# Kernel optimization log

Measured on AMD Instinct MI355X. Metric: run time of the kernel, lower is better.

The kernel has to match this reference:

```python
import jax, jax.numpy as jnp
import numpy as np

EMBED = 1024
N_HEADS = 16
HEAD_DIM = EMBED // N_HEADS
B, T = 2, 2048


def setup_inputs() -> dict:
    key = jax.random.key(0)
    k1, k2, k3 = jax.random.split(key, 3)
    x = jax.random.normal(k1, (B, T, EMBED), dtype=jnp.float32)
    # torch nn.Linear(embed, 3*embed, bias=False): weight [3C, C]; store as [C, 3C] for x @ W
    w_attn = jax.random.normal(k2, (EMBED, 3 * EMBED), dtype=jnp.float32) * (EMBED ** -0.5)
    w_proj = jax.random.normal(k3, (EMBED, EMBED), dtype=jnp.float32) * (EMBED ** -0.5)
    return {"x": x, "w_attn": w_attn, "w_proj": w_proj}


def reference(x, w_attn, w_proj):
    Bb, Tt, C = x.shape
    kqv = x @ w_attn  # [B, T, 3C]
    # NOTE: original code unpacks as k, q, v (k first)
    k, q, v = jnp.split(kqv, 3, axis=2)
    def heads(t):
        return t.reshape(Bb, Tt, N_HEADS, HEAD_DIM).transpose(0, 2, 1, 3)  # [B, H, T, D]
    k, q, v = heads(k), heads(q), heads(v)
    scale = HEAD_DIM ** -0.5
    wei = jnp.einsum("bhqd,bhkd->bhqk", q, k) * scale  # [B, H, T, T]
    mask = jnp.tril(jnp.ones((Tt, Tt), dtype=bool))
    wei = jnp.where(mask[None, None], wei, -jnp.inf)
    wei = jax.nn.softmax(wei, axis=-1)
    y = jnp.einsum("bhqk,bhkd->bhqd", wei, v)  # [B, H, T, D]
    y = y.transpose(0, 2, 1, 3).reshape(Bb, Tt, C)
    return y @ w_proj
```

## Files before the change

### kernel.cpp

```cpp
#include <hip/hip_runtime.h>

typedef unsigned short u16;
typedef unsigned int u32;

typedef __attribute__((ext_vector_type(4))) float f32x4;
typedef __attribute__((ext_vector_type(8))) short s16x8;

__device__ __forceinline__ u16 f2bf(float f) {
    u32 u = __builtin_bit_cast(u32, f);
    u += 0x7fffu + ((u >> 16) & 1u);
    return (u16)(u >> 16);
}

__device__ __forceinline__ u32 pk_bf16(float a, float b) {
    return (u32)f2bf(a) | ((u32)f2bf(b) << 16);
}

__device__ __forceinline__ u32 cvtpk(float a, float b) {
    u32 r;
    asm("v_cvt_pk_bf16_f32 %0, %1, %2" : "=v"(r) : "v"(a), "v"(b));
    return r;
}

#if __has_builtin(__builtin_amdgcn_exp2f)
#define EXP2(x) __builtin_amdgcn_exp2f(x)
#else
#define EXP2(x) exp2f(x)
#endif

__device__ __forceinline__ void gload16(const u16* g, u16* l) {
    __builtin_amdgcn_global_load_lds(
        (const __attribute__((address_space(1))) void*)(const void*)g,
        (__attribute__((address_space(3))) void*)(void*)l, 16, 0, 0);
}

__global__ void k_cast(const float* __restrict__ in, u16* __restrict__ out) {
    int i = (blockIdx.x * 256 + threadIdx.x) * 4;
    float4 v = *(const float4*)(in + i);
    uint2 pk;
    pk.x = pk_bf16(v.x, v.y);
    pk.y = pk_bf16(v.z, v.w);
    *(uint2*)(out + i) = pk;
}

__global__ void k_transpose(const float* __restrict__ in, u16* __restrict__ out,
                            int K, int N) {
    __shared__ float tile[32][33];
    int n0 = blockIdx.x * 32, k0 = blockIdx.y * 32;
    int x = threadIdx.x, y = threadIdx.y;
#pragma unroll
    for (int j = 0; j < 32; j += 8)
        tile[y + j][x] = in[(size_t)(k0 + y + j) * N + n0 + x];
    __syncthreads();
#pragma unroll
    for (int j = 0; j < 32; j += 8)
        out[(size_t)(n0 + y + j) * K + k0 + x] = f2bf(tile[x][y + j]);
}

template <int EPI>
__global__ __launch_bounds__(256, 2) void k_gemm(
        const u16* __restrict__ A, const u16* __restrict__ Bt,
        void* __restrict__ Cout, u16* __restrict__ Vt, int N, int K) {
    __shared__ u16 As[128 * 32];
    __shared__ u16 Bs[128 * 32];
    const int nbn = N >> 7;
    const int bm = (int)blockIdx.x / nbn, bn = (int)blockIdx.x % nbn;
    const int tid = threadIdx.x;
    const int wv = tid >> 6, ln = tid & 63;
    const int lg = ln >> 4, lr = ln & 15;
    const int wr = (wv >> 1) << 6, wc = (wv & 1) << 6;

    const u16* gA = A + (size_t)(bm * 128 + wv * 32 + (ln >> 2)) * K + (ln & 3) * 8;
    const u16* gB = Bt + (size_t)(bn * 128 + wv * 32 + (ln >> 2)) * K + (ln & 3) * 8;
    u16* lA = As + wv * 1024;
    u16* lB = Bs + wv * 1024;

    f32x4 acc[4][4] = {};

    for (int k0 = 0; k0 < K; k0 += 32) {
        gload16(gA + k0, lA);
        gload16(gA + k0 + 16 * K, lA + 512);
        gload16(gB + k0, lB);
        gload16(gB + k0 + 16 * K, lB + 512);
        __syncthreads();
        s16x8 af[4], bf[4];
#pragma unroll
        for (int mi = 0; mi < 4; ++mi)
            af[mi] = *(const s16x8*)&As[(wr + mi * 16 + lr) * 32 + lg * 8];
#pragma unroll
        for (int ni = 0; ni < 4; ++ni)
            bf[ni] = *(const s16x8*)&Bs[(wc + ni * 16 + lr) * 32 + lg * 8];
#pragma unroll
        for (int mi = 0; mi < 4; ++mi)
#pragma unroll
            for (int ni = 0; ni < 4; ++ni)
                acc[mi][ni] = __builtin_amdgcn_mfma_f32_16x16x32_bf16(
                        af[mi], bf[ni], acc[mi][ni], 0, 0, 0);
        __syncthreads();
    }

    const int crow0 = bm * 128 + wr + lg * 4;
    const int ccol0 = bn * 128 + wc + lr;
    if (EPI == 0) {
        float* Co = (float*)Cout;
#pragma unroll
        for (int mi = 0; mi < 4; ++mi)
#pragma unroll
            for (int ni = 0; ni < 4; ++ni)
#pragma unroll
                for (int r = 0; r < 4; ++r)
                    Co[(size_t)(crow0 + mi * 16 + r) * N + ccol0 + ni * 16] =
                            acc[mi][ni][r];
    } else {
        if (bn < 16) {
            const float qs = (bn >= 8) ? 0.18033688011112042f : 1.0f;
            u16* Co = (u16*)Cout;
#pragma unroll
            for (int mi = 0; mi < 4; ++mi)
#pragma unroll
                for (int ni = 0; ni < 4; ++ni)
#pragma unroll
                    for (int r = 0; r < 4; ++r)
                        Co[(size_t)(crow0 + mi * 16 + r) * 3072 + ccol0 + ni * 16] =
                                f2bf(acc[mi][ni][r] * qs);
        } else {
#pragma unroll
            for (int mi = 0; mi < 4; ++mi) {
                int row = crow0 + mi * 16;
                int bb = row >> 11, t = row & 2047;
#pragma unroll
                for (int ni = 0; ni < 4; ++ni) {
                    int hd = ccol0 + ni * 16 - 2048;
                    uint2 pk;
                    pk.x = pk_bf16(acc[mi][ni][0], acc[mi][ni][1]);
                    pk.y = pk_bf16(acc[mi][ni][2], acc[mi][ni][3]);
                    *(uint2*)&Vt[(size_t)(bb * 1024 + hd) * 2048 + t] = pk;
                }
            }
        }
    }
}

__global__ __launch_bounds__(256, 2) void k_attn(
        const u16* __restrict__ kqv, const u16* __restrict__ Vt,
        u16* __restrict__ y) {
    const int orig = blockIdx.x;
    const int xcd = orig & 7, slot = orig >> 3;
    const int bh = xcd * 4 + (slot >> 4);
    const int qp = slot & 15;
    const int b = bh >> 4, h = bh & 15;
    const int tid = threadIdx.x;
    const int wave = tid >> 6, lane = tid & 63;
    const int lg = lane >> 4, lr = lane & 15;

    __shared__ u16 Ks[2][64 * 72];
    __shared__ u16 Vs[2][64 * 72];
    __shared__ u16 Ps[4][16 * 64];

    const u16* Kg = kqv + (size_t)b * 2048 * 3072 + h * 64;
    const u16* Qg = Kg + 1024;
    const u16* Vg = Vt + (size_t)bh * 64 * 2048;

    const int srow = tid >> 2, ssl = tid & 3;
    const int soff = srow * 72 + ssl * 8;
    const u16* kgp = Kg + (size_t)srow * 3072 + ssl * 8;
    const u16* vgp = Vg + (size_t)srow * 2048 + ssl * 8;

    s16x8 ones;
#pragma unroll
    for (int i = 0; i < 8; ++i) ones[i] = (short)0x3F80;

    for (int pass = 0; pass < 2; ++pass) {
        const int qt = pass ? (31 - qp) : qp;
        const int nkt = qt + 1;
        const int qbase = qt * 64 + wave * 16;

        const u16* qrp = Qg + (size_t)(qbase + lr) * 3072;
        const s16x8 qf0 = *(const s16x8*)(qrp + lg * 8);
        const s16x8 qf1 = *(const s16x8*)(qrp + 32 + lg * 8);

        f32x4 o[4] = {};
        f32x4 l4 = {};

        uint4 ka0 = *(const uint4*)(kgp);
        uint4 ka1 = *(const uint4*)(kgp + 32);
        uint4 va0 = *(const uint4*)(vgp);
        uint4 va1 = *(const uint4*)(vgp + 32);
        *(uint4*)&Ks[0][soff] = ka0;
        *(uint4*)&Ks[0][soff + 32] = ka1;
        *(uint4*)&Vs[0][soff] = va0;
        *(uint4*)&Vs[0][soff + 32] = va1;

        for (int kt = 0; kt < nkt; ++kt) {
            const int cur = kt & 1;
            __syncthreads();
            const bool more = (kt + 1) < nkt;
            if (more) {
                const u16* kn = kgp + (size_t)(kt + 1) * 64 * 3072;
                const u16* vn = vgp + (kt + 1) * 64;
                ka0 = *(const uint4*)(kn);
                ka1 = *(const uint4*)(kn + 32);
                va0 = *(const uint4*)(vn);
                va1 = *(const uint4*)(vn + 32);
            }

            f32x4 st[4];
#pragma unroll
            for (int kb = 0; kb < 4; ++kb) {
                s16x8 kf0 = *(const s16x8*)&Ks[cur][(kb * 16 + lr) * 72 + lg * 8];
                s16x8 kf1 = *(const s16x8*)&Ks[cur][(kb * 16 + lr) * 72 + 32 + lg * 8];
                f32x4 z = {};
                z = __builtin_amdgcn_mfma_f32_16x16x32_bf16(kf0, qf0, z, 0, 0, 0);
                z = __builtin_amdgcn_mfma_f32_16x16x32_bf16(kf1, qf1, z, 0, 0, 0);
                st[kb] = z;
            }

            if (kt == nkt - 1) {
                const int q_abs = qbase + lr;
                const int kb0 = kt * 64 + lg * 4;
#pragma unroll
                for (int kb = 0; kb < 4; ++kb)
#pragma unroll
                    for (int r = 0; r < 4; ++r)
                        st[kb][r] = EXP2((kb0 + kb * 16 + r <= q_abs)
                                             ? st[kb][r] : -3e38f);
            } else {
#pragma unroll
                for (int kb = 0; kb < 4; ++kb)
#pragma unroll
                    for (int r = 0; r < 4; ++r) st[kb][r] = EXP2(st[kb][r]);
            }

#pragma unroll
            for (int kb = 0; kb < 4; ++kb) {
                const int kbs = (kb + lr) & 3;
                uint2 w;
                w.x = cvtpk(st[kb][0], st[kb][1]);
                w.y = cvtpk(st[kb][2], st[kb][3]);
                *(uint2*)&Ps[wave][lr * 64 + kbs * 16 + lg * 4] = w;
            }
            asm volatile("s_waitcnt lgkmcnt(0)" ::: "memory");
            __builtin_amdgcn_sched_barrier(0);

#pragma unroll
            for (int half = 0; half < 2; ++half) {
                const int kbs = ((half * 2 + (lg >> 1)) + lr) & 3;
                s16x8 pf = *(const s16x8*)&Ps[wave][lr * 64 + kbs * 16 + (lg & 1) * 8];
                l4 = __builtin_amdgcn_mfma_f32_16x16x32_bf16(ones, pf, l4, 0, 0, 0);
#pragma unroll
                for (int dt = 0; dt < 4; ++dt) {
                    s16x8 vf = *(const s16x8*)&Vs[cur][(dt * 16 + lr) * 72 + half * 32 + lg * 8];
                    o[dt] = __builtin_amdgcn_mfma_f32_16x16x32_bf16(vf, pf, o[dt], 0, 0, 0);
                }
            }

            if (more) {
                *(uint4*)&Ks[cur ^ 1][soff] = ka0;
                *(uint4*)&Ks[cur ^ 1][soff + 32] = ka1;
                *(uint4*)&Vs[cur ^ 1][soff] = va0;
                *(uint4*)&Vs[cur ^ 1][soff + 32] = va1;
            }
        }
        __syncthreads();

        const float inv = 1.0f / l4[0];
        u16* yb = y + (size_t)(b * 2048 + qbase + lr) * 1024 + h * 64;
#pragma unroll
        for (int dt = 0; dt < 4; ++dt) {
            uint2 w;
            w.x = cvtpk(o[dt][0] * inv, o[dt][1] * inv);
            w.y = cvtpk(o[dt][2] * inv, o[dt][3] * inv);
            *(uint2*)(yb + dt * 16 + lg * 4) = w;
        }
    }
}

extern "C" void kernel_launch(void* const* d_in, const int* in_sizes, int n_in,
                              void* d_out, int out_size, void* d_ws, size_t ws_size,
                              hipStream_t stream) {
    const float* x = (const float*)d_in[0];
    const float* w_attn = (const float*)d_in[1];
    const float* w_proj = (const float*)d_in[2];
    float* out = (float*)d_out;
    char* ws = (char*)d_ws;

    u16* x_bf = (u16*)(ws);
    u16* wat  = (u16*)(ws + (size_t)(8 << 20));
    u16* wpt  = (u16*)(ws + (size_t)(14 << 20));
    u16* kqv  = (u16*)(ws + (size_t)(16 << 20));
    u16* vt   = (u16*)(ws + (size_t)(40 << 20));
    u16* yb   = (u16*)(ws + (size_t)(48 << 20));

    k_cast<<<4096, 256, 0, stream>>>(x, x_bf);
    k_transpose<<<dim3(96, 32), dim3(32, 8), 0, stream>>>(w_attn, wat, 1024, 3072);
    k_transpose<<<dim3(32, 32), dim3(32, 8), 0, stream>>>(w_proj, wpt, 1024, 1024);
    k_gemm<1><<<32 * 24, 256, 0, stream>>>(x_bf, wat, kqv, vt, 3072, 1024);
    k_attn<<<512, 256, 0, stream>>>(kqv, vt, yb);
    k_gemm<0><<<32 * 8, 256, 0, stream>>>(yb, wpt, out, nullptr, 1024, 1024);
}
```

Measured before the change: 182.2 us.

## Use direct global-to-LDS async loads with XOR swizzle and one q-tile per block

The attention kernel now stages K and V tiles with global_load_lds directly into XOR-swizzled LDS tiles, dropping the register round-trip and the padded layout. Each block handles a single query tile instead of a balanced pair, so the grid doubles and launch bounds allow 4 blocks per CU. Wave priority is raised around the MFMA sections, and the P buffer gets a finer swizzle. The cost is less load balance per block, since causal work is no longer paired inside a block and relies on the scheduler instead. The exp2 builtin is also replaced by exp2f.

```diff
diff --git a/kernel.cpp b/kernel.cpp
--- a/kernel.cpp
+++ b/kernel.cpp
@@ -5,6 +5,7 @@
 
 typedef __attribute__((ext_vector_type(4))) float f32x4;
 typedef __attribute__((ext_vector_type(8))) short s16x8;
+typedef __attribute__((ext_vector_type(4))) short s16x4;
 
 __device__ __forceinline__ u16 f2bf(float f) {
     u32 u = __builtin_bit_cast(u32, f);
@@ -22,11 +23,7 @@
     return r;
 }
 
-#if __has_builtin(__builtin_amdgcn_exp2f)
-#define EXP2(x) __builtin_amdgcn_exp2f(x)
-#else
 #define EXP2(x) exp2f(x)
-#endif
 
 __device__ __forceinline__ void gload16(const u16* g, u16* l) {
     __builtin_amdgcn_global_load_lds(
@@ -141,137 +138,140 @@
     }
 }
 
-__global__ __launch_bounds__(256, 2) void k_attn(
+__global__ __launch_bounds__(256, 4) void k_attn(
         const u16* __restrict__ kqv, const u16* __restrict__ Vt,
         u16* __restrict__ y) {
     const int orig = blockIdx.x;
     const int xcd = orig & 7, slot = orig >> 3;
-    const int bh = xcd * 4 + (slot >> 4);
-    const int qp = slot & 15;
+    const int bh = xcd * 4 + (slot >> 5);
+    const int qs = slot & 31;
+    const int qt = (qs & 1) ? (31 - (qs >> 1)) : (qs >> 1);
     const int b = bh >> 4, h = bh & 15;
     const int tid = threadIdx.x;
     const int wave = tid >> 6, lane = tid & 63;
     const int lg = lane >> 4, lr = lane & 15;
 
-    __shared__ u16 Ks[2][64 * 72];
-    __shared__ u16 Vs[2][64 * 72];
+    __shared__ u16 Ks[2][64 * 64];
+    __shared__ u16 Vs[2][64 * 64];
     __shared__ u16 Ps[4][16 * 64];
 
     const u16* Kg = kqv + (size_t)b * 2048 * 3072 + h * 64;
     const u16* Qg = Kg + 1024;
     const u16* Vg = Vt + (size_t)bh * 64 * 2048;
 
-    const int srow = tid >> 2, ssl = tid & 3;
-    const int soff = srow * 72 + ssl * 8;
-    const u16* kgp = Kg + (size_t)srow * 3072 + ssl * 8;
-    const u16* vgp = Vg + (size_t)srow * 2048 + ssl * 8;
+    const int srow = wave * 16 + (lane >> 3);
+    const int cK = (lane & 7) ^ (lane >> 3);
+    const u16* kg0 = Kg + (size_t)srow * 3072 + cK * 8;
+    const u16* vg0 = Vg + (size_t)srow * 2048 + cK * 8;
+
+    const int nkt = qt + 1;
+    const int qbase = qt * 64 + wave * 16;
+
+    const u16* qrp = Qg + (size_t)(qbase + lr) * 3072;
+    const s16x8 qf0 = *(const s16x8*)(qrp + lg * 8);
+    const s16x8 qf1 = *(const s16x8*)(qrp + 32 + lg * 8);
 
     s16x8 ones;
 #pragma unroll
     for (int i = 0; i < 8; ++i) ones[i] = (short)0x3F80;
 
-    for (int pass = 0; pass < 2; ++pass) {
-        const int qt = pass ? (31 - qp) : qp;
-        const int nkt = qt + 1;
-        const int qbase = qt * 64 + wave * 16;
-
-        const u16* qrp = Qg + (size_t)(qbase + lr) * 3072;
-        const s16x8 qf0 = *(const s16x8*)(qrp + lg * 8);
-        const s16x8 qf1 = *(const s16x8*)(qrp + 32 + lg * 8);
-
-        f32x4 o[4] = {};
-        f32x4 l4 = {};
-
-        uint4 ka0 = *(const uint4*)(kgp);
-        uint4 ka1 = *(const uint4*)(kgp + 32);
-        uint4 va0 = *(const uint4*)(vgp);
-        uint4 va1 = *(const uint4*)(vgp + 32);
-        *(uint4*)&Ks[0][soff] = ka0;
-        *(uint4*)&Ks[0][soff + 32] = ka1;
-        *(uint4*)&Vs[0][soff] = va0;
-        *(uint4*)&Vs[0][soff + 32] = va1;
-
-        for (int kt = 0; kt < nkt; ++kt) {
-            const int cur = kt & 1;
-            __syncthreads();
-            const bool more = (kt + 1) < nkt;
-            if (more) {
-                const u16* kn = kgp + (size_t)(kt + 1) * 64 * 3072;
-                const u16* vn = vgp + (kt + 1) * 64;
-                ka0 = *(const uint4*)(kn);
-                ka1 = *(const uint4*)(kn + 32);
-                va0 = *(const uint4*)(vn);
-                va1 = *(const uint4*)(vn + 32);
+    f32x4 o[4] = {};
+    f32x4 l4 = {};
+
+    u16* Psw = &Ps[wave][0];
+    const int swz = (lr & 7);
+
+#define STAGE(bb, t)                                            \
+    {                                                           \
+        const u16* kp_ = kg0 + (size_t)(t) * 64 * 3072;         \
+        const u16* vp_ = vg0 + (size_t)(t) * 64;                \
+        u16* lk_ = &Ks[bb][wave * 1024];                        \
+        u16* lv_ = &Vs[bb][wave * 1024];                        \
+        gload16(kp_, lk_);                                      \
+        gload16(kp_ + 8 * 3072, lk_ + 512);                     \
+        gload16(vp_, lv_);                                      \
+        gload16(vp_ + 8 * 2048, lv_ + 512);                     \
+    }
+
+    STAGE(0, 0);
+    asm volatile("s_waitcnt vmcnt(0)\n\ts_barrier" ::: "memory");
+
+    for (int kt = 0; kt < nkt; ++kt) {
+        const int cur = kt & 1;
+        if (kt + 1 < nkt) STAGE(cur ^ 1, kt + 1);
+
+        f32x4 st[4];
+        __builtin_amdgcn_s_setprio(1);
+#pragma unroll
+        for (int kb = 0; kb < 4; ++kb) {
+            const int row = kb * 16 + lr;
+            s16x8 kf0 = *(const s16x8*)&Ks[cur][row * 64 + ((lg ^ swz) << 3)];
+            s16x8 kf1 = *(const s16x8*)&Ks[cur][row * 64 + (((4 + lg) ^ swz) << 3)];
+            f32x4 z = {};
+            z = __builtin_amdgcn_mfma_f32_16x16x32_bf16(kf0, qf0, z, 0, 0, 0);
+            z = __builtin_amdgcn_mfma_f32_16x16x32_bf16(kf1, qf1, z, 0, 0, 0);
+            st[kb] = z;
+        }
+        __builtin_amdgcn_s_setprio(0);
+
+        if (kt == nkt - 1) {
+            const int q_abs = qbase + lr;
+            const int kb0 = kt * 64 + lg * 4;
+#pragma unroll
+            for (int kb = 0; kb < 4; ++kb)
+#pragma unroll
+                for (int r = 0; r < 4; ++r)
+                    st[kb][r] = EXP2((kb0 + kb * 16 + r <= q_abs)
+                                         ? st[kb][r] : -3e38f);
+        } else {
+#pragma unroll
+            for (int kb = 0; kb < 4; ++kb)
+#pragma unroll
+                for (int r = 0; r < 4; ++r) st[kb][r] = EXP2(st[kb][r]);
+        }
+
+#pragma unroll
+        for (int kb = 0; kb < 4; ++kb) {
+            const int sw = (kb * 4 + lg + lr) & 15;
+            uint2 w;
+            w.x = cvtpk(st[kb][0], st[kb][1]);
+            w.y = cvtpk(st[kb][2], st[kb][3]);
+            *(uint2*)&Psw[lr * 64 + sw * 4] = w;
+        }
+        asm volatile("s_waitcnt lgkmcnt(0)" ::: "memory");
+        __builtin_amdgcn_sched_barrier(0);
+
+        __builtin_amdgcn_s_setprio(1);
+#pragma unroll
+        for (int half = 0; half < 2; ++half) {
+            const int s0 = (half * 8 + lg * 2 + lr) & 15;
+            const int s1 = (half * 8 + lg * 2 + 1 + lr) & 15;
+            s16x4 pa = *(const s16x4*)&Psw[lr * 64 + s0 * 4];
+            s16x4 pb = *(const s16x4*)&Psw[lr * 64 + s1 * 4];
+            s16x8 pf = __builtin_shufflevector(pa, pb, 0, 1, 2, 3, 4, 5, 6, 7);
+            l4 = __builtin_amdgcn_mfma_f32_16x16x32_bf16(ones, pf, l4, 0, 0, 0);
+#pragma unroll
+            for (int dt = 0; dt < 4; ++dt) {
+                const int vrow = dt * 16 + lr;
+                s16x8 vf = *(const s16x8*)&Vs[cur][vrow * 64 +
+                                                   (((half * 4 + lg) ^ swz) << 3)];
+                o[dt] = __builtin_amdgcn_mfma_f32_16x16x32_bf16(vf, pf, o[dt], 0, 0, 0);
             }
-
-            f32x4 st[4];
-#pragma unroll
-            for (int kb = 0; kb < 4; ++kb) {
-                s16x8 kf0 = *(const s16x8*)&Ks[cur][(kb * 16 + lr) * 72 + lg * 8];
-                s16x8 kf1 = *(const s16x8*)&Ks[cur][(kb * 16 + lr) * 72 + 32 + lg * 8];
-                f32x4 z = {};
-                z = __builtin_amdgcn_mfma_f32_16x16x32_bf16(kf0, qf0, z, 0, 0, 0);
-                z = __builtin_amdgcn_mfma_f32_16x16x32_bf16(kf1, qf1, z, 0, 0, 0);
-                st[kb] = z;
-            }
-
-            if (kt == nkt - 1) {
-                const int q_abs = qbase + lr;
-                const int kb0 = kt * 64 + lg * 4;
-#pragma unroll
-                for (int kb = 0; kb < 4; ++kb)
-#pragma unroll
-                    for (int r = 0; r < 4; ++r)
-                        st[kb][r] = EXP2((kb0 + kb * 16 + r <= q_abs)
-                                             ? st[kb][r] : -3e38f);
-            } else {
-#pragma unroll
-                for (int kb = 0; kb < 4; ++kb)
-#pragma unroll
-                    for (int r = 0; r < 4; ++r) st[kb][r] = EXP2(st[kb][r]);
-            }
-
-#pragma unroll
-            for (int kb = 0; kb < 4; ++kb) {
-                const int kbs = (kb + lr) & 3;
-                uint2 w;
-                w.x = cvtpk(st[kb][0], st[kb][1]);
-                w.y = cvtpk(st[kb][2], st[kb][3]);
-                *(uint2*)&Ps[wave][lr * 64 + kbs * 16 + lg * 4] = w;
-            }
-            asm volatile("s_waitcnt lgkmcnt(0)" ::: "memory");
-            __builtin_amdgcn_sched_barrier(0);
-
-#pragma unroll
-            for (int half = 0; half < 2; ++half) {
-                const int kbs = ((half * 2 + (lg >> 1)) + lr) & 3;
-                s16x8 pf = *(const s16x8*)&Ps[wave][lr * 64 + kbs * 16 + (lg & 1) * 8];
-                l4 = __builtin_amdgcn_mfma_f32_16x16x32_bf16(ones, pf, l4, 0, 0, 0);
-#pragma unroll
-                for (int dt = 0; dt < 4; ++dt) {
-                    s16x8 vf = *(const s16x8*)&Vs[cur][(dt * 16 + lr) * 72 + half * 32 + lg * 8];
-                    o[dt] = __builtin_amdgcn_mfma_f32_16x16x32_bf16(vf, pf, o[dt], 0, 0, 0);
-                }
-            }
-
-            if (more) {
-                *(uint4*)&Ks[cur ^ 1][soff] = ka0;
-                *(uint4*)&Ks[cur ^ 1][soff + 32] = ka1;
-                *(uint4*)&Vs[cur ^ 1][soff] = va0;
-                *(uint4*)&Vs[cur ^ 1][soff + 32] = va1;
-            }
-        }
-        __syncthreads();
-
-        const float inv = 1.0f / l4[0];
-        u16* yb = y + (size_t)(b * 2048 + qbase + lr) * 1024 + h * 64;
-#pragma unroll
-        for (int dt = 0; dt < 4; ++dt) {
-            uint2 w;
-            w.x = cvtpk(o[dt][0] * inv, o[dt][1] * inv);
-            w.y = cvtpk(o[dt][2] * inv, o[dt][3] * inv);
-            *(uint2*)(yb + dt * 16 + lg * 4) = w;
-        }
+        }
+        __builtin_amdgcn_s_setprio(0);
+
+        asm volatile("s_waitcnt vmcnt(0)\n\ts_barrier" ::: "memory");
+    }
+#undef STAGE
+
+    const float inv = 1.0f / l4[0];
+    u16* yb = y + (size_t)(b * 2048 + qbase + lr) * 1024 + h * 64;
+#pragma unroll
+    for (int dt = 0; dt < 4; ++dt) {
+        uint2 w;
+        w.x = cvtpk(o[dt][0] * inv, o[dt][1] * inv);
+        w.y = cvtpk(o[dt][2] * inv, o[dt][3] * inv);
+        *(uint2*)(yb + dt * 16 + lg * 4) = w;
     }
 }
 
@@ -295,6 +295,6 @@
     k_transpose<<<dim3(96, 32), dim3(32, 8), 0, stream>>>(w_attn, wat, 1024, 3072);
     k_transpose<<<dim3(32, 32), dim3(32, 8), 0, stream>>>(w_proj, wpt, 1024, 1024);
     k_gemm<1><<<32 * 24, 256, 0, stream>>>(x_bf, wat, kqv, vt, 3072, 1024);
-    k_attn<<<512, 256, 0, stream>>>(kqv, vt, yb);
+    k_attn<<<1024, 256, 0, stream>>>(kqv, vt, yb);
     k_gemm<0><<<32 * 8, 256, 0, stream>>>(yb, wpt, out, nullptr, 1024, 1024);
 }
```

Result: slower. 201.7 us (+10.7%).
